# Optimization experiments

Measured on AMD Instinct MI355X. Metric: run time of the kernel, lower is better.

The kernel has to match this reference:

```python
import jax, jax.numpy as jnp
import numpy as np
from jax import lax

L, B, N, D = 6, 4, 2048, 512
H, DH = 8, 64
ID = H * DH           # 512
M = 266               # int(64*log(64)) random features
INNER = 2 * D         # conformer expansion
K = 31                # depthwise kernel
PAD = (15, 15)        # calc_same_padding(31)
EPS_LN = 1e-5


def setup_inputs() -> dict:
    key = jax.random.key(0)
    ks = jax.random.split(key, 12)
    s = 0.02
    return {
        "x": jax.random.normal(ks[0], (B, N, D), jnp.float32),
        "ln1_g": jnp.ones((L, D), jnp.float32),
        "ln1_b": jnp.zeros((L, D), jnp.float32),
        "wq": jax.random.normal(ks[1], (L, ID, D), jnp.float32) * s,
        "bq": jnp.zeros((L, ID), jnp.float32),
        "wk": jax.random.normal(ks[2], (L, ID, D), jnp.float32) * s,
        "bk": jnp.zeros((L, ID), jnp.float32),
        "wv": jax.random.normal(ks[3], (L, ID, D), jnp.float32) * s,
        "bv": jnp.zeros((L, ID), jnp.float32),
        "wo": jax.random.normal(ks[4], (L, ID, D), jnp.float32) * s,
        "bo": jnp.zeros((L, D), jnp.float32),
        # FAVOR+ random projection buffer (gaussian orthogonal ~ iid gaussian rows)
        "proj": jax.random.normal(ks[5], (L, M, DH), jnp.float32),
        "ln2_g": jnp.ones((L, D), jnp.float32),
        "ln2_b": jnp.zeros((L, D), jnp.float32),
        "pw1_w": jax.random.normal(ks[6], (L, 2 * INNER, D), jnp.float32) * s,
        "pw1_b": jnp.zeros((L, 2 * INNER), jnp.float32),
        "dw_w": jax.random.normal(ks[7], (L, INNER, K), jnp.float32) * s,
        "dw_b": jnp.zeros((L, INNER), jnp.float32),
        "pw2_w": jax.random.normal(ks[8], (L, D, INNER), jnp.float32) * s,
        "pw2_b": jnp.zeros((L, D), jnp.float32),
    }


def layer_norm(x, g, b):
    mu = jnp.mean(x, axis=-1, keepdims=True)
    var = jnp.mean((x - mu) ** 2, axis=-1, keepdims=True)
    return (x - mu) * lax.rsqrt(var + EPS_LN) * g + b


def softmax_kernel(data, proj, is_query, eps=1e-4):
    # data: [b,h,n,dh], proj: [m,dh]
    dn = DH ** -0.25
    ratio = M ** -0.5
    data_dash = jnp.einsum('bhnd,md->bhnm', dn * data, proj)
    diag = jnp.sum(data * data, axis=-1, keepdims=True) * 0.5 * dn * dn  # [b,h,n,1]
    if is_query:
        mx = jnp.max(data_dash, axis=-1, keepdims=True)
        return ratio * (jnp.exp(data_dash - diag - mx) + eps)
    else:
        return ratio * jnp.exp(data_dash - diag + eps)


def favor_attention(q, k, v, proj):
    qp = softmax_kernel(q, proj, True)   # [b,h,n,m]
    kp = softmax_kernel(k, proj, False)  # [b,h,n,m]
    k_cumsum = jnp.sum(kp, axis=-2)      # [b,h,m]
    d_inv = 1.0 / (jnp.einsum('bhnm,bhm->bhn', qp, k_cumsum) + 1e-8)
    context = jnp.einsum('bhnm,bhne->bhme', kp, v)          # [b,h,m,dh]
    out = jnp.einsum('bhme,bhnm,bhn->bhne', context, qp, d_inv)
    return out


def pcmer_forward(x, ln1_g, ln1_b, wq, bq, wk, bk, wv, bv, wo, bo, proj,
                  ln2_g, ln2_b, pw1_w, pw1_b, dw_w, dw_b, pw2_w, pw2_b):
    for l in range(L):
        # --- self attention (FAVOR+) ---
        h = layer_norm(x, ln1_g[l], ln1_b[l])
        q = (h @ wq[l].T + bq[l]).reshape(B, N, H, DH).transpose(0, 2, 1, 3)
        k = (h @ wk[l].T + bk[l]).reshape(B, N, H, DH).transpose(0, 2, 1, 3)
        v = (h @ wv[l].T + bv[l]).reshape(B, N, H, DH).transpose(0, 2, 1, 3)
        o = favor_attention(q, k, v, proj[l])                 # [b,h,n,dh]
        o = o.transpose(0, 2, 1, 3).reshape(B, N, ID)
        x = x + (o @ wo[l].T + bo[l])
        # --- conformer conv module ---
        h = layer_norm(x, ln2_g[l], ln2_b[l])
        y = h @ pw1_w[l].T + pw1_b[l]                         # [b,n,2*inner]
        a, g = y[..., :INNER], y[..., INNER:]
        y = a * jax.nn.sigmoid(g)                             # GLU
        yt = jnp.pad(y.transpose(0, 2, 1), ((0, 0), (0, 0), PAD))  # [b,inner,n+30]
        dw = lax.conv_general_dilated(
            yt, dw_w[l][:, None, :], window_strides=(1,), padding='VALID',
            feature_group_count=INNER,
            dimension_numbers=('NCH', 'OIH', 'NCH')) + dw_b[l][None, :, None]
        dw = jax.nn.silu(dw).transpose(0, 2, 1)               # [b,n,inner]
        x = x + (dw @ pw2_w[l].T + pw2_b[l])
    return x


def reference(x, ln1_g, ln1_b, wq, bq, wk, bk, wv, bv, wo, bo, proj,
              ln2_g, ln2_b, pw1_w, pw1_b, dw_w, dw_b, pw2_w, pw2_b):
    return pcmer_forward(x, ln1_g, ln1_b, wq, bq, wk, bk, wv, bv, wo, bo, proj,
                         ln2_g, ln2_b, pw1_w, pw1_b, dw_w, dw_b, pw2_w, pw2_b)
```

## Files before the change

kernel.cpp:

```cpp
#include <hip/hip_runtime.h>


#define L_LAYERS 6
#define B_ 4
#define N_ 2048
#define D_ 512
#define H_ 8
#define DH_ 64
#define M_ 266
#define INNER_ 1024
#define T_ 8192
#define PS_ 320
#define QKVS_ 1536
#define NS_ 8

typedef __attribute__((ext_vector_type(8))) short short8;
typedef __attribute__((ext_vector_type(4))) float floatx4;

__device__ __forceinline__ ushort f2bf(float f) {
  union { float f; uint u; } v; v.f = f;
  uint r = v.u + 0x7fffu + ((v.u >> 16) & 1u);
  return (ushort)(r >> 16);
}
__device__ __forceinline__ float bf2f(ushort u) {
  union { uint u; float f; } v; v.u = ((uint)u) << 16;
  return v.f;
}
__device__ __forceinline__ float wave_sum(float v) {
#pragma unroll
  for (int m = 1; m < 64; m <<= 1) v += __shfl_xor(v, m);
  return v;
}
__device__ __forceinline__ void async_cp16(const void* g, void* l) {
  __builtin_amdgcn_global_load_lds(
      (const __attribute__((address_space(1))) void*)g,
      (__attribute__((address_space(3))) void*)l, 16, 0, 0);
}

__global__ void f2bf4_kernel(const float4* __restrict__ in, ushort* __restrict__ out, int n4) {
  int i = blockIdx.x * 256 + threadIdx.x;
  if (i < n4) {
    float4 v = in[i];
    ushort4 r;
    r.x = f2bf(v.x); r.y = f2bf(v.y); r.z = f2bf(v.z); r.w = f2bf(v.w);
    *(ushort4*)(out + (size_t)i * 4) = r;
  }
}
__global__ void pack_qkv_w(const float4* __restrict__ src, ushort* __restrict__ dst, int off) {
  int i = blockIdx.x * 256 + threadIdx.x;
  if (i >= L_LAYERS * 512 * 128) return;
  int l = i >> 16;
  int rem = i & 65535;
  int row = rem >> 7, c4 = rem & 127;
  float4 v = src[i];
  ushort4 r;
  r.x = f2bf(v.x); r.y = f2bf(v.y); r.z = f2bf(v.z); r.w = f2bf(v.w);
  *(ushort4*)(dst + ((size_t)l * QKVS_ + off + row) * 512 + c4 * 4) = r;
}
__global__ void pack_qkv_b(const float* __restrict__ bq, const float* __restrict__ bk,
                           const float* __restrict__ bv, float* __restrict__ dst) {
  int i = blockIdx.x * 256 + threadIdx.x;
  if (i >= L_LAYERS * QKVS_) return;
  int l = i / QKVS_, c = i % QKVS_;
  dst[i] = c < 512 ? bq[l * 512 + c] : (c < 1024 ? bk[l * 512 + c - 512] : bv[l * 512 + c - 1024]);
}
__global__ void pad_proj(const float* __restrict__ proj, ushort* __restrict__ dst) {
  int i = blockIdx.x * 256 + threadIdx.x;
  if (i >= L_LAYERS * 320 * 64) return;
  int l = i / (320 * 64), rem = i % (320 * 64), m = rem >> 6, kk = rem & 63;
  dst[i] = (m < M_) ? f2bf(proj[((size_t)l * M_ + m) * 64 + kk]) : (ushort)0;
}
__global__ void pack_pw1_w(const float4* __restrict__ src, ushort* __restrict__ dst) {
  int i = blockIdx.x * 256 + threadIdx.x;
  if (i >= L_LAYERS * 2048 * 128) return;
  int l = i >> 18;
  int rem = i & 262143;
  int cp = rem >> 7, c4 = rem & 127;
  int s = (cp >> 4) & 1;
  int srow = ((cp >> 5) << 4) + (cp & 15) + s * 1024;
  float4 v = src[((size_t)l * 2048 + srow) * 128 + c4];
  ushort4 r;
  r.x = f2bf(v.x); r.y = f2bf(v.y); r.z = f2bf(v.z); r.w = f2bf(v.w);
  *(ushort4*)(dst + ((size_t)l * 2048 + cp) * 512 + c4 * 4) = r;
}
__global__ void pack_pw1_b(const float* __restrict__ src, float* __restrict__ dst) {
  int i = blockIdx.x * 256 + threadIdx.x;
  if (i >= L_LAYERS * 2048) return;
  int l = i >> 11, cp = i & 2047;
  int s = (cp >> 4) & 1;
  int srow = ((cp >> 5) << 4) + (cp & 15) + s * 1024;
  dst[i] = src[l * 2048 + srow];
}

__global__ __launch_bounds__(256) void ln_kernel(const float* __restrict__ x,
                                                 const float* __restrict__ g,
                                                 const float* __restrict__ b,
                                                 ushort* __restrict__ out) {
  const int t = blockIdx.x;
  const int tid = threadIdx.x;
  const float* row = x + (size_t)t * D_;
  float v0 = row[tid], v1 = row[tid + 256];
  float s1 = v0 + v1;
  float s2 = v0 * v0 + v1 * v1;
  s1 = wave_sum(s1);
  s2 = wave_sum(s2);
  __shared__ float sh1[4], sh2[4];
  int w = tid >> 6;
  if ((tid & 63) == 0) { sh1[w] = s1; sh2[w] = s2; }
  __syncthreads();
  s1 = sh1[0] + sh1[1] + sh1[2] + sh1[3];
  s2 = sh2[0] + sh2[1] + sh2[2] + sh2[3];
  float mu = s1 * (1.f / D_);
  float var = s2 * (1.f / D_) - mu * mu;
  float rs = rsqrtf(var + 1e-5f);
  out[(size_t)t * D_ + tid]       = f2bf((v0 - mu) * rs * g[tid] + b[tid]);
  out[(size_t)t * D_ + tid + 256] = f2bf((v1 - mu) * rs * g[tid + 256] + b[tid + 256]);
}

template <bool HAS_RES, bool OUT_BF16, int ACT, int KT>
__global__ __launch_bounds__(256) void gemm_mfma(const ushort* __restrict__ A,
                                                 const ushort* __restrict__ W,
                                                 const float* __restrict__ bias,
                                                 const float* __restrict__ res,
                                                 void* __restrict__ Cout,
                                                 int ldc) {
  constexpr int NT = KT / 32;
  __shared__ ushort As[3][128 * 32];
  __shared__ ushort Bs[3][128 * 32];
  const int tid = threadIdx.x;
  const int w = tid >> 6, lane = tid & 63;
  const int row0 = blockIdx.x * 128, col0 = blockIdx.y * 128;
  const int rl = lane >> 2;
  const int lc = ((lane & 3) ^ ((lane >> 3) & 3)) * 8;
  const ushort* gA0 = A + (size_t)(row0 + w * 32 + rl) * KT + lc;
  const ushort* gA1 = gA0 + (size_t)16 * KT;
  const ushort* gB0 = W + (size_t)(col0 + w * 32 + rl) * KT + lc;
  const ushort* gB1 = gB0 + (size_t)16 * KT;
  const int m16 = lane & 15, quad = lane >> 4;
  const int awr = (w >> 1) * 64, bwc = (w & 1) * 64;
  floatx4 acc[4][4] = {};

  auto stage = [&](int t, int buf) {
    async_cp16(gA0 + t * 32, As[buf] + w * 1024);
    async_cp16(gA1 + t * 32, As[buf] + w * 1024 + 512);
    async_cp16(gB0 + t * 32, Bs[buf] + w * 1024);
    async_cp16(gB1 + t * 32, Bs[buf] + w * 1024 + 512);
  };
  auto body = [&](int buf, bool bar2) {
    short8 af[4], bfr[4];
#pragma unroll
    for (int i = 0; i < 4; i++) {
      int r = awr + i * 16 + m16;
      af[i] = *(const short8*)&As[buf][r * 32 + (quad ^ ((r >> 1) & 3)) * 8];
    }
#pragma unroll
    for (int j = 0; j < 4; j++) {
      int r = bwc + j * 16 + m16;
      bfr[j] = *(const short8*)&Bs[buf][r * 32 + (quad ^ ((r >> 1) & 3)) * 8];
    }
    if (bar2) {
      asm volatile("s_waitcnt lgkmcnt(0)" ::: "memory");
      __builtin_amdgcn_sched_barrier(0);
      __builtin_amdgcn_s_barrier();
    }
#pragma unroll
    for (int i = 0; i < 4; i++)
#pragma unroll
      for (int j = 0; j < 4; j++)
        acc[i][j] = __builtin_amdgcn_mfma_f32_16x16x32_bf16(af[i], bfr[j], acc[i][j], 0, 0, 0);
  };

  stage(0, 0);
  stage(1, 1);
  int c = 0;
  for (int t = 0; t < NT - 2; t++) {
    int pf = c + 2; if (pf >= 3) pf -= 3;
    stage(t + 2, pf);
    asm volatile("s_waitcnt vmcnt(8)" ::: "memory");
    __builtin_amdgcn_s_barrier();
    body(c, true);
    c++; if (c >= 3) c -= 3;
  }
  asm volatile("s_waitcnt vmcnt(4)" ::: "memory");
  __builtin_amdgcn_s_barrier();
  body(c, false);
  c++; if (c >= 3) c -= 3;
  asm volatile("s_waitcnt vmcnt(0)" ::: "memory");
  __builtin_amdgcn_s_barrier();
  body(c, false);

  if (ACT == 0) {
#pragma unroll
    for (int i = 0; i < 4; i++) {
      const int r0 = row0 + awr + i * 16 + quad * 4;
#pragma unroll
      for (int j = 0; j < 4; j++) {
        const int cc = col0 + bwc + j * 16 + m16;
        const float bv = bias[cc];
#pragma unroll
        for (int r = 0; r < 4; r++) {
          float vv = acc[i][j][r] + bv;
          if (HAS_RES) vv += res[(size_t)(r0 + r) * ldc + cc];
          if (OUT_BF16) ((ushort*)Cout)[(size_t)(r0 + r) * ldc + cc] = f2bf(vv);
          else          ((float*)Cout)[(size_t)(r0 + r) * ldc + cc] = vv;
        }
      }
    }
  } else {
#pragma unroll
    for (int i = 0; i < 4; i++) {
      const int r0 = row0 + awr + i * 16 + quad * 4;
#pragma unroll
      for (int jp = 0; jp < 2; jp++) {
        const int j = jp * 2;
        const int ca = col0 + bwc + j * 16 + m16;
        const float ba = bias[ca], bg = bias[ca + 16];
        const int oc = ((col0 + bwc) >> 1) + jp * 16 + m16;
#pragma unroll
        for (int r = 0; r < 4; r++) {
          float a = acc[i][j][r] + ba;
          float g = acc[i][j + 1][r] + bg;
          float z = a / (1.f + expf(-g));
          ((ushort*)Cout)[(size_t)(r0 + r) * ldc + oc] = f2bf(z);
        }
      }
    }
  }
}

template <bool OUT_BF16, int ACT, int KT>
__global__ __launch_bounds__(256, 2) void gemm_big(const ushort* __restrict__ A,
                                                   const ushort* __restrict__ W,
                                                   const float* __restrict__ bias,
                                                   void* __restrict__ Cout,
                                                   int ldc) {
  constexpr int NT = KT / 32;
  __shared__ ushort As[3][256 * 32];
  __shared__ ushort Bs[3][128 * 32];
  const int tid = threadIdx.x;
  const int w = tid >> 6, lane = tid & 63;
  const int row0 = blockIdx.x * 256, col0 = blockIdx.y * 128;
  const int rl = lane >> 2;
  const int lc = ((lane & 3) ^ ((lane >> 3) & 3)) * 8;
  const ushort* gA = A + (size_t)(row0 + w * 64 + rl) * KT + lc;
  const ushort* gB = W + (size_t)(col0 + w * 32 + rl) * KT + lc;
  const int m16 = lane & 15, quad = lane >> 4;
  const int awr = (w >> 1) * 128;
  const int bwc = (w & 1) * 64;
  floatx4 acc[8][4] = {};

  auto stage = [&](int t, int buf) {
#pragma unroll
    for (int j = 0; j < 4; j++)
      async_cp16(gA + ((size_t)j * 16) * KT + t * 32, As[buf] + w * 2048 + j * 512);
#pragma unroll
    for (int j = 0; j < 2; j++)
      async_cp16(gB + ((size_t)j * 16) * KT + t * 32, Bs[buf] + w * 1024 + j * 512);
  };
  auto body = [&](int buf, bool bar2) {
    short8 af[8], bfr[4];
#pragma unroll
    for (int i = 0; i < 8; i++) {
      int r = awr + i * 16 + m16;
      af[i] = *(const short8*)&As[buf][r * 32 + (quad ^ ((r >> 1) & 3)) * 8];
    }
#pragma unroll
    for (int j = 0; j < 4; j++) {
      int r = bwc + j * 16 + m16;
      bfr[j] = *(const short8*)&Bs[buf][r * 32 + (quad ^ ((r >> 1) & 3)) * 8];
    }
    if (bar2) {
      asm volatile("s_waitcnt lgkmcnt(0)" ::: "memory");
      __builtin_amdgcn_sched_barrier(0);
      __builtin_amdgcn_s_barrier();
    }
#pragma unroll
    for (int i = 0; i < 8; i++)
#pragma unroll
      for (int j = 0; j < 4; j++)
        acc[i][j] = __builtin_amdgcn_mfma_f32_16x16x32_bf16(af[i], bfr[j], acc[i][j], 0, 0, 0);
  };

  stage(0, 0);
  stage(1, 1);
  int c = 0;
  for (int t = 0; t < NT - 2; t++) {
    int pf = c + 2; if (pf >= 3) pf -= 3;
    stage(t + 2, pf);
    asm volatile("s_waitcnt vmcnt(12)" ::: "memory");
    __builtin_amdgcn_s_barrier();
    body(c, true);
    c++; if (c >= 3) c -= 3;
  }
  asm volatile("s_waitcnt vmcnt(6)" ::: "memory");
  __builtin_amdgcn_s_barrier();
  body(c, false);
  c++; if (c >= 3) c -= 3;
  asm volatile("s_waitcnt vmcnt(0)" ::: "memory");
  __builtin_amdgcn_s_barrier();
  body(c, false);

  if (ACT == 0) {
#pragma unroll
    for (int i = 0; i < 8; i++) {
      const int r0 = row0 + awr + i * 16 + quad * 4;
#pragma unroll
      for (int j = 0; j < 4; j++) {
        const int cc = col0 + bwc + j * 16 + m16;
        const float bv = bias[cc];
#pragma unroll
        for (int r = 0; r < 4; r++) {
          float vv = acc[i][j][r] + bv;
          if (OUT_BF16) ((ushort*)Cout)[(size_t)(r0 + r) * ldc + cc] = f2bf(vv);
          else          ((float*)Cout)[(size_t)(r0 + r) * ldc + cc] = vv;
        }
      }
    }
  } else {
#pragma unroll
    for (int i = 0; i < 8; i++) {
      const int r0 = row0 + awr + i * 16 + quad * 4;
#pragma unroll
      for (int jp = 0; jp < 2; jp++) {
        const int j = jp * 2;
        const int ca = col0 + bwc + j * 16 + m16;
        const float ba = bias[ca], bg = bias[ca + 16];
        const int oc = ((col0 + bwc) >> 1) + jp * 16 + m16;
#pragma unroll
        for (int r = 0; r < 4; r++) {
          float a = acc[i][j][r] + ba;
          float g = acc[i][j + 1][r] + bg;
          float z = a / (1.f + expf(-g));
          ((ushort*)Cout)[(size_t)(r0 + r) * ldc + oc] = f2bf(z);
        }
      }
    }
  }
}

__global__ __launch_bounds__(256) void ctx_phi_mfma(const ushort* __restrict__ qkv,
                                                    const ushort* __restrict__ projp,
                                                    float* __restrict__ part,
                                                    float* __restrict__ kpart) {
  __shared__ ushort projs[64 * 64];
  __shared__ ushort kts[32 * 64];
  __shared__ ushort kps[64][40];
  __shared__ ushort vsT[64][40];
  __shared__ float diag_sh[32];
  __shared__ float kshare[4][64];
  const int bh = blockIdx.x, mt = blockIdx.y, ns = blockIdx.z;
  const int b = bh >> 3, h = bh & 7;
  const int m0 = mt * 64;
  const int tid = threadIdx.x;
  const int w = tid >> 6, lane = tid & 63, l16 = lane & 15, quad = lane >> 4;
  const int rl8 = lane >> 3;
  const int lc8 = ((lane & 7) ^ (rl8 & 7)) * 8;
#pragma unroll
  for (int j = 0; j < 2; j++) {
    const int rb = w * 16 + j * 8;
    async_cp16(projp + (size_t)(m0 + rb + rl8) * 64 + lc8, projs + rb * 64);
  }
  const int nn = tid >> 3;
  const int a8 = tid & 7;
  const int gn = nn >> 3, jn = nn & 7;
  const int pc = ((gn ^ (a8 & 3)) << 3) | jn;
  const int km = tid & 63, kg = tid >> 6;
  const float dn = 0.35355339059327373f;
  const float ratio = 0.06131393394849658f;
  floatx4 acc[4] = {};
  float ksp = 0.f;
  for (int nstep = 0; nstep < 2048 / NS_ / 32; nstep++) {
    const int n0 = ns * (2048 / NS_) + nstep * 32;
    {
      const int rb = w * 8;
      async_cp16(qkv + (size_t)(b * N_ + n0 + rb + rl8) * QKVS_ + 512 + h * 64 + lc8,
                 kts + rb * 64);
    }
    uint4 vv = *(const uint4*)(qkv + ((size_t)(b * N_ + n0 + nn)) * QKVS_ + 1024 + h * 64 + a8 * 8);
    __syncthreads();
    {
      const int r = tid >> 3;
      const int c = tid & 7;
      short8 kv8 = *(const short8*)&kts[r * 64 + c * 8];
      const ushort* u = (const ushort*)&kv8;
      float s = 0.f;
#pragma unroll
      for (int j = 0; j < 8; j++) { float f = bf2f(u[j]); s += f * f; }
      s += __shfl_xor(s, 1);
      s += __shfl_xor(s, 2);
      s += __shfl_xor(s, 4);
      if ((tid & 7) == 0) diag_sh[r] = 0.0625f * s;
    }
    {
      const ushort* ve = (const ushort*)&vv;
#pragma unroll
      for (int j = 0; j < 8; j++) vsT[a8 * 8 + j][pc] = ve[j];
    }
    __syncthreads();
    floatx4 pacc[2] = {};
#pragma unroll
    for (int s = 0; s < 2; s++) {
      const int ar = w * 16 + l16;
      short8 af = *(const short8*)&projs[ar * 64 + ((s * 4 + quad) ^ (ar & 7)) * 8];
#pragma unroll
      for (int nj = 0; nj < 2; nj++) {
        const int br = nj * 16 + l16;
        short8 bf = *(const short8*)&kts[br * 64 + ((s * 4 + quad) ^ (br & 7)) * 8];
        pacc[nj] = __builtin_amdgcn_mfma_f32_16x16x32_bf16(af, bf, pacc[nj], 0, 0, 0);
      }
    }
#pragma unroll
    for (int nj = 0; nj < 2; nj++) {
      const int n = nj * 16 + l16;
      const float dgn = diag_sh[n];
#pragma unroll
      for (int r = 0; r < 4; r++) {
        const int m = w * 16 + quad * 4 + r;
        float val = (m0 + m < M_) ? ratio * expf(dn * pacc[nj][r] - dgn + 1e-4f) : 0.f;
        kps[m][(((n >> 3) ^ ((m >> 3) & 3)) << 3) | (n & 7)] = f2bf(val);
      }
    }
    __syncthreads();
    const int am = w * 16 + l16;
    const int apg = quad ^ ((am >> 3) & 3);
    short8 af = *(const short8*)&kps[am][apg * 8];
#pragma unroll
    for (int et = 0; et < 4; et++) {
      const int be = et * 16 + l16;
      const int bpg = quad ^ ((be >> 3) & 3);
      short8 bf = *(const short8*)&vsT[be][bpg * 8];
      acc[et] = __builtin_amdgcn_mfma_f32_16x16x32_bf16(af, bf, acc[et], 0, 0, 0);
    }
    {
      short8 kr = *(const short8*)&kps[km][kg * 8];
      const ushort* ku = (const ushort*)&kr;
#pragma unroll
      for (int j = 0; j < 8; j++) ksp += bf2f(ku[j]);
    }
  }
  float* pb = part + ((size_t)(bh * NS_ + ns) * 5 + mt) * 4096;
#pragma unroll
  for (int et = 0; et < 4; et++)
#pragma unroll
    for (int r = 0; r < 4; r++)
      pb[(w * 16 + quad * 4 + r) * 64 + et * 16 + l16] = acc[et][r];
  kshare[kg][km] = ksp;
  __syncthreads();
  if (tid < 64)
    kpart[((size_t)(bh * NS_ + ns) * 5 + mt) * 64 + tid] =
        kshare[0][tid] + kshare[1][tid] + kshare[2][tid] + kshare[3][tid];
}

__global__ __launch_bounds__(256) void ctx_reduce(const float* __restrict__ part,
                                                  const float* __restrict__ kpart,
                                                  ushort* __restrict__ ctxbT,
                                                  float* __restrict__ ksum) {
  const int bh = blockIdx.x, mt = blockIdx.y;
  const int tid = threadIdx.x;
  const int w = tid >> 6, lane = tid & 63;
  for (int oc = w; oc < 8; oc += 4) {
    const int mbase = mt * 64 + oc * 8;
    if (mbase < 288) {
      float s[8] = {0.f, 0.f, 0.f, 0.f, 0.f, 0.f, 0.f, 0.f};
#pragma unroll
      for (int ns = 0; ns < NS_; ns++) {
        const float* pb = part + ((size_t)(bh * NS_ + ns) * 5 + mt) * 4096;
#pragma unroll
        for (int ml = 0; ml < 8; ml++) s[ml] += pb[(oc * 8 + ml) * 64 + lane];
      }
      ushort tmp[8];
#pragma unroll
      for (int ml = 0; ml < 8; ml++) tmp[ml] = f2bf(s[ml]);
      *(short8*)(ctxbT + ((size_t)(bh * 64 + lane)) * 288 + mbase) = *(const short8*)tmp;
    }
  }
  if (tid < 64) {
    float s = 0.f;
#pragma unroll
    for (int ns = 0; ns < NS_; ns++)
      s += kpart[((size_t)(bh * NS_ + ns) * 5 + mt) * 64 + tid];
    ksum[(size_t)bh * PS_ + mt * 64 + tid] = s;
  }
}

__global__ __launch_bounds__(256, 4) void attn_fused(const ushort* __restrict__ qkv,
                                                     const ushort* __restrict__ projp,
                                                     const ushort* __restrict__ ctxbT,
                                                     const float* __restrict__ ksum,
                                                     ushort* __restrict__ o) {
  __shared__ __align__(16) ushort sm[14336];
  __shared__ float ks_sh[288];
  __shared__ float diag_sh[64];
  ushort* As = sm;
  ushort* Bs = sm + 4096;
  ushort (*qst)[40] = (ushort(*)[40])sm;
  const int bh = blockIdx.x, b = bh >> 3, h = bh & 7;
  const int n0 = blockIdx.y * 64;
  const int tid = threadIdx.x;
  const int w = tid >> 6, lane = tid & 63, l16 = lane & 15, quad = lane >> 4;
  const int rl8 = lane >> 3;
  const int lc8 = ((lane & 7) ^ (rl8 & 7)) * 8;
#pragma unroll
  for (int j = 0; j < 2; j++) {
    const int rb = w * 16 + j * 8;
    async_cp16(qkv + (size_t)(b * N_ + n0 + rb + rl8) * QKVS_ + h * 64 + lc8, As + rb * 64);
  }
#pragma unroll
  for (int j = 0; j < 5; j++) {
    const int rb = w * 40 + j * 8;
    async_cp16(projp + (size_t)(rb + rl8) * 64 + lc8, Bs + rb * 64);
  }
  for (int i = tid; i < 288; i += 256) ks_sh[i] = ksum[(size_t)bh * PS_ + i];
  __syncthreads();
  {
    const int r = w * 16 + (lane >> 2);
    const int c0 = 2 * (lane & 3);
    float s = 0.f;
#pragma unroll
    for (int cc = 0; cc < 2; cc++) {
      short8 vv = *(const short8*)&As[r * 64 + ((c0 + cc) ^ (r & 7)) * 8];
      const ushort* u = (const ushort*)&vv;
#pragma unroll
      for (int j = 0; j < 8; j++) { float f = bf2f(u[j]); s += f * f; }
    }
    s += __shfl_xor(s, 1);
    s += __shfl_xor(s, 2);
    if ((lane & 3) == 0) diag_sh[r] = 0.0625f * s;
  }
  __syncthreads();
  float dgr[4];
#pragma unroll
  for (int r = 0; r < 4; r++) dgr[r] = diag_sh[w * 16 + quad * 4 + r];
  floatx4 acc[18];
#pragma unroll
  for (int cf = 0; cf < 18; cf++) acc[cf] = (floatx4){0.f, 0.f, 0.f, 0.f};
  const int ar = w * 16 + l16;
#pragma unroll
  for (int s = 0; s < 2; s++) {
    short8 af = *(const short8*)&As[ar * 64 + ((s * 4 + quad) ^ (ar & 7)) * 8];
#pragma unroll
    for (int cf = 0; cf < 10; cf++) {
      const int br = cf * 16 + l16;
      short8 bf = *(const short8*)&Bs[br * 64 + ((s * 4 + quad) ^ (br & 7)) * 8];
      acc[cf] = __builtin_amdgcn_mfma_f32_16x16x32_bf16(af, bf, acc[cf], 0, 0, 0);
    }
  }
  __syncthreads();
#pragma unroll
  for (int j = 0; j < 4; j++) {
    const int rb = w * 32 + j * 8;
    async_cp16(projp + (size_t)(160 + rb + rl8) * 64 + lc8, Bs + rb * 64);
  }
  __syncthreads();
#pragma unroll
  for (int s = 0; s < 2; s++) {
    short8 af = *(const short8*)&As[ar * 64 + ((s * 4 + quad) ^ (ar & 7)) * 8];
#pragma unroll
    for (int cf = 10; cf < 18; cf++) {
      const int br = (cf - 10) * 16 + l16;
      short8 bf = *(const short8*)&Bs[br * 64 + ((s * 4 + quad) ^ (br & 7)) * 8];
      acc[cf] = __builtin_amdgcn_mfma_f32_16x16x32_bf16(af, bf, acc[cf], 0, 0, 0);
    }
  }
  const float dn = 0.35355339059327373f;
  const float ratio = 0.06131393394849658f;
  float mxr[4];
#pragma unroll
  for (int r = 0; r < 4; r++) {
    float mx = -1e30f;
#pragma unroll
    for (int cf = 0; cf < 18; cf++) {
      const int col = cf * 16 + l16;
      if (col < M_) mx = fmaxf(mx, dn * acc[cf][r]);
    }
    mx = fmaxf(mx, __shfl_xor(mx, 1));
    mx = fmaxf(mx, __shfl_xor(mx, 2));
    mx = fmaxf(mx, __shfl_xor(mx, 4));
    mx = fmaxf(mx, __shfl_xor(mx, 8));
    mxr[r] = mx;
  }
  __syncthreads();
  float dacc[4] = {0.f, 0.f, 0.f, 0.f};
  floatx4 acc2[4] = {};
  const ushort* ctxrow = ctxbT + (size_t)bh * (64 * 288);
  for (int m0 = 0; m0 < 288; m0 += 32) {
    const int cf0 = m0 >> 4;
#pragma unroll
    for (int cc = 0; cc < 2; cc++) {
      const int col = m0 + cc * 16 + l16;
      const float kv = ks_sh[col];
#pragma unroll
      for (int r = 0; r < 4; r++) {
        float val = (col < M_) ? ratio * (expf(dn * acc[cf0 + cc][r] - dgr[r] - mxr[r]) + 1e-4f)
                               : 0.f;
        qst[w * 16 + quad * 4 + r][cc * 16 + l16] = f2bf(val);
        dacc[r] += val * kv;
      }
    }
    short8 af = *(const short8*)&qst[w * 16 + l16][quad * 8];
#pragma unroll
    for (int et = 0; et < 4; et++) {
      short8 bf = *(const short8*)(ctxrow + (size_t)(et * 16 + l16) * 288 + m0 + quad * 8);
      acc2[et] = __builtin_amdgcn_mfma_f32_16x16x32_bf16(af, bf, acc2[et], 0, 0, 0);
    }
  }
  float di[4];
#pragma unroll
  for (int r = 0; r < 4; r++) {
    float d = dacc[r];
    d += __shfl_xor(d, 1);
    d += __shfl_xor(d, 2);
    d += __shfl_xor(d, 4);
    d += __shfl_xor(d, 8);
    di[r] = 1.f / (d + 1e-8f);
  }
#pragma unroll
  for (int r = 0; r < 4; r++) {
    const int n = n0 + w * 16 + quad * 4 + r;
#pragma unroll
    for (int et = 0; et < 4; et++)
      o[((size_t)(b * N_ + n)) * 512 + h * 64 + et * 16 + l16] = f2bf(acc2[et][r] * di[r]);
  }
}

#define TN_ 32
__global__ __launch_bounds__(256) void dwconv_kernel(const ushort* __restrict__ x,
                                                     const float* __restrict__ w,
                                                     const float* __restrict__ bias,
                                                     ushort* __restrict__ out) {
  const int bid = blockIdx.x;
  const int cb = bid & 3;
  const int nb = (bid >> 2) & (N_ / TN_ - 1);
  const int b  = bid >> 8;
  const int c = cb * 256 + threadIdx.x;
  const int n0 = nb * TN_;
  float win[TN_ + 30];
#pragma unroll
  for (int i = 0; i < TN_ + 30; i++) {
    int nn = n0 + i - 15;
    win[i] = (nn >= 0 && nn < N_) ? bf2f(x[(size_t)(b * N_ + nn) * INNER_ + c]) : 0.f;
  }
  float wc[31];
#pragma unroll
  for (int kk = 0; kk < 31; kk++) wc[kk] = w[c * 31 + kk];
  const float bsv = bias[c];
#pragma unroll
  for (int j = 0; j < TN_; j++) {
    float acc = bsv;
#pragma unroll
    for (int kk = 0; kk < 31; kk++) acc += win[j + kk] * wc[kk];
    acc = acc / (1.f + expf(-acc));
    out[(size_t)(b * N_ + n0 + j) * INNER_ + c] = f2bf(acc);
  }
}

extern "C" void kernel_launch(void* const* d_in, const int* in_sizes, int n_in,
                              void* d_out, int out_size, void* d_ws, size_t ws_size,
                              hipStream_t stream) {
  const float* in_x  = (const float*)d_in[0];
  const float* ln1_g = (const float*)d_in[1];
  const float* ln1_b = (const float*)d_in[2];
  const float* wq    = (const float*)d_in[3];
  const float* bq    = (const float*)d_in[4];
  const float* wk    = (const float*)d_in[5];
  const float* bk    = (const float*)d_in[6];
  const float* wv    = (const float*)d_in[7];
  const float* bv    = (const float*)d_in[8];
  const float* wo    = (const float*)d_in[9];
  const float* bo    = (const float*)d_in[10];
  const float* proj  = (const float*)d_in[11];
  const float* ln2_g = (const float*)d_in[12];
  const float* ln2_b = (const float*)d_in[13];
  const float* pw1_w = (const float*)d_in[14];
  const float* pw1_b = (const float*)d_in[15];
  const float* dw_w  = (const float*)d_in[16];
  const float* dw_b  = (const float*)d_in[17];
  const float* pw2_w = (const float*)d_in[18];
  const float* pw2_b = (const float*)d_in[19];

  char* cur = (char*)d_ws;
  auto alloc = [&](size_t bytes) { char* p = cur; cur += (bytes + 255) & ~(size_t)255; return p; };
  float*  x    = (float*)alloc((size_t)T_ * D_ * 4);
  ushort* p    = (ushort*)alloc((size_t)T_ * INNER_ * 2 * 2);
  float*  part = (float*)alloc((size_t)32 * NS_ * 5 * 4096 * 4);
  float*  kpart= (float*)alloc((size_t)32 * NS_ * 5 * 64 * 4);
  ushort* ctxb = (ushort*)alloc((size_t)32 * 288 * 64 * 2);
  float*  ksum = (float*)alloc((size_t)32 * PS_ * 4);
  ushort* h    = (ushort*)alloc((size_t)T_ * D_ * 2);
  ushort* qkv  = (ushort*)alloc((size_t)T_ * QKVS_ * 2);
  ushort* obuf = (ushort*)alloc((size_t)T_ * D_ * 2);
  ushort* wqkv_b = (ushort*)alloc((size_t)L_LAYERS * QKVS_ * 512 * 2);
  float*  bqkv   = (float*)alloc((size_t)L_LAYERS * QKVS_ * 4);
  ushort* wo_b = (ushort*)alloc((size_t)L_LAYERS * D_ * D_ * 2);
  ushort* pjp  = (ushort*)alloc((size_t)L_LAYERS * 320 * 64 * 2);
  ushort* p1_b = (ushort*)alloc((size_t)L_LAYERS * 2048 * D_ * 2);
  float*  pb1  = (float*)alloc((size_t)L_LAYERS * 2048 * 4);
  ushort* p2_b = (ushort*)alloc((size_t)L_LAYERS * D_ * INNER_ * 2);
  ushort* glu  = p;
  ushort* conv = p + (size_t)T_ * INNER_;

  pack_qkv_w<<<(L_LAYERS * 512 * 128 + 255) / 256, 256, 0, stream>>>((const float4*)wq, wqkv_b, 0);
  pack_qkv_w<<<(L_LAYERS * 512 * 128 + 255) / 256, 256, 0, stream>>>((const float4*)wk, wqkv_b, 512);
  pack_qkv_w<<<(L_LAYERS * 512 * 128 + 255) / 256, 256, 0, stream>>>((const float4*)wv, wqkv_b, 1024);
  pack_qkv_b<<<(L_LAYERS * QKVS_ + 255) / 256, 256, 0, stream>>>(bq, bk, bv, bqkv);
  pad_proj<<<(L_LAYERS * 320 * 64 + 255) / 256, 256, 0, stream>>>(proj, pjp);
  pack_pw1_w<<<(L_LAYERS * 2048 * 128 + 255) / 256, 256, 0, stream>>>((const float4*)pw1_w, p1_b);
  pack_pw1_b<<<(L_LAYERS * 2048 + 255) / 256, 256, 0, stream>>>(pw1_b, pb1);
  {
    int n4 = L_LAYERS * D_ * D_ / 4;
    f2bf4_kernel<<<(n4 + 255) / 256, 256, 0, stream>>>((const float4*)wo, wo_b, n4);
    n4 = L_LAYERS * D_ * INNER_ / 4;
    f2bf4_kernel<<<(n4 + 255) / 256, 256, 0, stream>>>((const float4*)pw2_w, p2_b, n4);
  }

  for (int l = 0; l < L_LAYERS; l++) {
    const ushort* wqkvl = wqkv_b + (size_t)l * QKVS_ * 512;
    const ushort* wol = wo_b + (size_t)l * D_ * D_;
    const ushort* pjl = pjp + (size_t)l * 320 * 64;
    const ushort* p1l = p1_b + (size_t)l * 2048 * D_;
    const ushort* p2l = p2_b + (size_t)l * D_ * INNER_;
    const float*  dwl = dw_w + (size_t)l * INNER_ * 31;
    const float*  dwbl = dw_b + (size_t)l * INNER_;
    const float*  xin = (l == 0) ? in_x : x;
    float* xout = (l == L_LAYERS - 1) ? (float*)d_out : x;

    ln_kernel<<<T_, 256, 0, stream>>>(xin, ln1_g + l * D_, ln1_b + l * D_, h);
    gemm_big<true, 0, 512><<<dim3(T_ / 256, QKVS_ / 128), 256, 0, stream>>>(
        h, wqkvl, bqkv + (size_t)l * QKVS_, qkv, QKVS_);
    ctx_phi_mfma<<<dim3(32, 5, NS_), 256, 0, stream>>>(qkv, pjl, part, kpart);
    ctx_reduce<<<dim3(32, 5), 256, 0, stream>>>(part, kpart, ctxb, ksum);
    attn_fused<<<dim3(32, 32), 256, 0, stream>>>(qkv, pjl, ctxb, ksum, obuf);
    gemm_mfma<true, false, 0, 512><<<dim3(T_ / 128, 4), 256, 0, stream>>>(
        obuf, wol, bo + l * D_, xin, x, D_);
    ln_kernel<<<T_, 256, 0, stream>>>(x, ln2_g + l * D_, ln2_b + l * D_, h);
    gemm_big<true, 1, 512><<<dim3(T_ / 256, 16), 256, 0, stream>>>(
        h, p1l, pb1 + (size_t)l * 2048, glu, INNER_);
    dwconv_kernel<<<B_ * (N_ / TN_) * 4, 256, 0, stream>>>(glu, dwl, dwbl, conv);
    gemm_mfma<true, false, 0, 1024><<<dim3(T_ / 128, 4), 256, 0, stream>>>(
        conv, p2l, pw2_b + l * D_, x, xout, D_);
  }
}
```

Measured before the change: 1.225 ms.

## Use smaller-tile GEMM for N=512 outputs, XCD swizzle, setprio, fused packing kernels

```diff
diff --git a/kernel.cpp b/kernel.cpp
--- a/kernel.cpp
+++ b/kernel.cpp
@@ -36,39 +36,59 @@
       (const __attribute__((address_space(1))) void*)g,
       (__attribute__((address_space(3))) void*)l, 16, 0, 0);
 }
-
-__global__ void f2bf4_kernel(const float4* __restrict__ in, ushort* __restrict__ out, int n4) {
+__device__ __forceinline__ int xcd_swz(int bid, int n) {
+  return (bid & 7) * (n >> 3) + (bid >> 3);
+}
+
+__global__ void f2bf4_dual(const float4* __restrict__ s1, int n1,
+                           const float4* __restrict__ s2, int n2,
+                           ushort* __restrict__ out) {
   int i = blockIdx.x * 256 + threadIdx.x;
-  if (i < n4) {
-    float4 v = in[i];
-    ushort4 r;
-    r.x = f2bf(v.x); r.y = f2bf(v.y); r.z = f2bf(v.z); r.w = f2bf(v.w);
-    *(ushort4*)(out + (size_t)i * 4) = r;
-  }
-}
-__global__ void pack_qkv_w(const float4* __restrict__ src, ushort* __restrict__ dst, int off) {
-  int i = blockIdx.x * 256 + threadIdx.x;
-  if (i >= L_LAYERS * 512 * 128) return;
-  int l = i >> 16;
-  int rem = i & 65535;
-  int row = rem >> 7, c4 = rem & 127;
-  float4 v = src[i];
+  if (i >= n1 + n2) return;
+  float4 v = (i < n1) ? s1[i] : s2[i - n1];
   ushort4 r;
   r.x = f2bf(v.x); r.y = f2bf(v.y); r.z = f2bf(v.z); r.w = f2bf(v.w);
-  *(ushort4*)(dst + ((size_t)l * QKVS_ + off + row) * 512 + c4 * 4) = r;
-}
-__global__ void pack_qkv_b(const float* __restrict__ bq, const float* __restrict__ bk,
-                           const float* __restrict__ bv, float* __restrict__ dst) {
+  *(ushort4*)(out + (size_t)i * 4) = r;
+}
+__global__ void pack_qkv_w3(const float4* __restrict__ wq, const float4* __restrict__ wk,
+                            const float4* __restrict__ wv, ushort* __restrict__ dst) {
   int i = blockIdx.x * 256 + threadIdx.x;
-  if (i >= L_LAYERS * QKVS_) return;
-  int l = i / QKVS_, c = i % QKVS_;
-  dst[i] = c < 512 ? bq[l * 512 + c] : (c < 1024 ? bk[l * 512 + c - 512] : bv[l * 512 + c - 1024]);
-}
-__global__ void pad_proj(const float* __restrict__ proj, ushort* __restrict__ dst) {
+  const int per = L_LAYERS * 512 * 128;
+  if (i >= 3 * per) return;
+  int seg = i / per;
+  int rem = i - seg * per;
+  const float4* src = seg == 0 ? wq : (seg == 1 ? wk : wv);
+  int l = rem >> 16;
+  int r2 = rem & 65535;
+  int row = r2 >> 7, c4 = r2 & 127;
+  float4 v = src[rem];
+  ushort4 r;
+  r.x = f2bf(v.x); r.y = f2bf(v.y); r.z = f2bf(v.z); r.w = f2bf(v.w);
+  *(ushort4*)(dst + ((size_t)l * QKVS_ + seg * 512 + row) * 512 + c4 * 4) = r;
+}
+__global__ void pack_small(const float* __restrict__ bq, const float* __restrict__ bk,
+                           const float* __restrict__ bv, float* __restrict__ bqkv,
+                           const float* __restrict__ proj, ushort* __restrict__ pjp,
+                           const float* __restrict__ pw1b, float* __restrict__ pb1) {
   int i = blockIdx.x * 256 + threadIdx.x;
-  if (i >= L_LAYERS * 320 * 64) return;
-  int l = i / (320 * 64), rem = i % (320 * 64), m = rem >> 6, kk = rem & 63;
-  dst[i] = (m < M_) ? f2bf(proj[((size_t)l * M_ + m) * 64 + kk]) : (ushort)0;
+  const int A = L_LAYERS * QKVS_;
+  const int Bn = L_LAYERS * 320 * 64;
+  const int C = L_LAYERS * 2048;
+  if (i < A) {
+    int l = i / QKVS_, c = i % QKVS_;
+    bqkv[i] = c < 512 ? bq[l * 512 + c]
+                      : (c < 1024 ? bk[l * 512 + c - 512] : bv[l * 512 + c - 1024]);
+  } else if (i < A + Bn) {
+    int j = i - A;
+    int l = j / (320 * 64), rem = j % (320 * 64), m = rem >> 6, kk = rem & 63;
+    pjp[j] = (m < M_) ? f2bf(proj[((size_t)l * M_ + m) * 64 + kk]) : (ushort)0;
+  } else if (i < A + Bn + C) {
+    int j = i - A - Bn;
+    int l = j >> 11, cp = j & 2047;
+    int s = (cp >> 4) & 1;
+    int srow = ((cp >> 5) << 4) + (cp & 15) + s * 1024;
+    pb1[j] = pw1b[l * 2048 + srow];
+  }
 }
 __global__ void pack_pw1_w(const float4* __restrict__ src, ushort* __restrict__ dst) {
   int i = blockIdx.x * 256 + threadIdx.x;
@@ -82,14 +102,6 @@
   ushort4 r;
   r.x = f2bf(v.x); r.y = f2bf(v.y); r.z = f2bf(v.z); r.w = f2bf(v.w);
   *(ushort4*)(dst + ((size_t)l * 2048 + cp) * 512 + c4 * 4) = r;
-}
-__global__ void pack_pw1_b(const float* __restrict__ src, float* __restrict__ dst) {
-  int i = blockIdx.x * 256 + threadIdx.x;
-  if (i >= L_LAYERS * 2048) return;
-  int l = i >> 11, cp = i & 2047;
-  int s = (cp >> 4) & 1;
-  int srow = ((cp >> 5) << 4) + (cp & 15) + s * 1024;
-  dst[i] = src[l * 2048 + srow];
 }
 
 __global__ __launch_bounds__(256) void ln_kernel(const float* __restrict__ x,
@@ -117,117 +129,6 @@
   out[(size_t)t * D_ + tid + 256] = f2bf((v1 - mu) * rs * g[tid + 256] + b[tid + 256]);
 }
 
-template <bool HAS_RES, bool OUT_BF16, int ACT, int KT>
-__global__ __launch_bounds__(256) void gemm_mfma(const ushort* __restrict__ A,
-                                                 const ushort* __restrict__ W,
-                                                 const float* __restrict__ bias,
-                                                 const float* __restrict__ res,
-                                                 void* __restrict__ Cout,
-                                                 int ldc) {
-  constexpr int NT = KT / 32;
-  __shared__ ushort As[3][128 * 32];
-  __shared__ ushort Bs[3][128 * 32];
-  const int tid = threadIdx.x;
-  const int w = tid >> 6, lane = tid & 63;
-  const int row0 = blockIdx.x * 128, col0 = blockIdx.y * 128;
-  const int rl = lane >> 2;
-  const int lc = ((lane & 3) ^ ((lane >> 3) & 3)) * 8;
-  const ushort* gA0 = A + (size_t)(row0 + w * 32 + rl) * KT + lc;
-  const ushort* gA1 = gA0 + (size_t)16 * KT;
-  const ushort* gB0 = W + (size_t)(col0 + w * 32 + rl) * KT + lc;
-  const ushort* gB1 = gB0 + (size_t)16 * KT;
-  const int m16 = lane & 15, quad = lane >> 4;
-  const int awr = (w >> 1) * 64, bwc = (w & 1) * 64;
-  floatx4 acc[4][4] = {};
-
-  auto stage = [&](int t, int buf) {
-    async_cp16(gA0 + t * 32, As[buf] + w * 1024);
-    async_cp16(gA1 + t * 32, As[buf] + w * 1024 + 512);
-    async_cp16(gB0 + t * 32, Bs[buf] + w * 1024);
-    async_cp16(gB1 + t * 32, Bs[buf] + w * 1024 + 512);
-  };
-  auto body = [&](int buf, bool bar2) {
-    short8 af[4], bfr[4];
-#pragma unroll
-    for (int i = 0; i < 4; i++) {
-      int r = awr + i * 16 + m16;
-      af[i] = *(const short8*)&As[buf][r * 32 + (quad ^ ((r >> 1) & 3)) * 8];
-    }
-#pragma unroll
-    for (int j = 0; j < 4; j++) {
-      int r = bwc + j * 16 + m16;
-      bfr[j] = *(const short8*)&Bs[buf][r * 32 + (quad ^ ((r >> 1) & 3)) * 8];
-    }
-    if (bar2) {
-      asm volatile("s_waitcnt lgkmcnt(0)" ::: "memory");
-      __builtin_amdgcn_sched_barrier(0);
-      __builtin_amdgcn_s_barrier();
-    }
-#pragma unroll
-    for (int i = 0; i < 4; i++)
-#pragma unroll
-      for (int j = 0; j < 4; j++)
-        acc[i][j] = __builtin_amdgcn_mfma_f32_16x16x32_bf16(af[i], bfr[j], acc[i][j], 0, 0, 0);
-  };
-
-  stage(0, 0);
-  stage(1, 1);
-  int c = 0;
-  for (int t = 0; t < NT - 2; t++) {
-    int pf = c + 2; if (pf >= 3) pf -= 3;
-    stage(t + 2, pf);
-    asm volatile("s_waitcnt vmcnt(8)" ::: "memory");
-    __builtin_amdgcn_s_barrier();
-    body(c, true);
-    c++; if (c >= 3) c -= 3;
-  }
-  asm volatile("s_waitcnt vmcnt(4)" ::: "memory");
-  __builtin_amdgcn_s_barrier();
-  body(c, false);
-  c++; if (c >= 3) c -= 3;
-  asm volatile("s_waitcnt vmcnt(0)" ::: "memory");
-  __builtin_amdgcn_s_barrier();
-  body(c, false);
-
-  if (ACT == 0) {
-#pragma unroll
-    for (int i = 0; i < 4; i++) {
-      const int r0 = row0 + awr + i * 16 + quad * 4;
-#pragma unroll
-      for (int j = 0; j < 4; j++) {
-        const int cc = col0 + bwc + j * 16 + m16;
-        const float bv = bias[cc];
-#pragma unroll
-        for (int r = 0; r < 4; r++) {
-          float vv = acc[i][j][r] + bv;
-          if (HAS_RES) vv += res[(size_t)(r0 + r) * ldc + cc];
-          if (OUT_BF16) ((ushort*)Cout)[(size_t)(r0 + r) * ldc + cc] = f2bf(vv);
-          else          ((float*)Cout)[(size_t)(r0 + r) * ldc + cc] = vv;
-        }
-      }
-    }
-  } else {
-#pragma unroll
-    for (int i = 0; i < 4; i++) {
-      const int r0 = row0 + awr + i * 16 + quad * 4;
-#pragma unroll
-      for (int jp = 0; jp < 2; jp++) {
-        const int j = jp * 2;
-        const int ca = col0 + bwc + j * 16 + m16;
-        const float ba = bias[ca], bg = bias[ca + 16];
-        const int oc = ((col0 + bwc) >> 1) + jp * 16 + m16;
-#pragma unroll
-        for (int r = 0; r < 4; r++) {
-          float a = acc[i][j][r] + ba;
-          float g = acc[i][j + 1][r] + bg;
-          float z = a / (1.f + expf(-g));
-          ((ushort*)Cout)[(size_t)(r0 + r) * ldc + oc] = f2bf(z);
-        }
-      }
-    }
-  }
-}
-
 template <bool OUT_BF16, int ACT, int KT>
 __global__ __launch_bounds__(256, 2) void gemm_big(const ushort* __restrict__ A,
                                                    const ushort* __restrict__ W,
@@ -239,7 +140,7 @@
   __shared__ ushort Bs[3][128 * 32];
   const int tid = threadIdx.x;
   const int w = tid >> 6, lane = tid & 63;
-  const int row0 = blockIdx.x * 256, col0 = blockIdx.y * 128;
+  const int row0 = xcd_swz(blockIdx.x, gridDim.x) * 256, col0 = blockIdx.y * 128;
   const int rl = lane >> 2;
   const int lc = ((lane & 3) ^ ((lane >> 3) & 3)) * 8;
   const ushort* gA = A + (size_t)(row0 + w * 64 + rl) * KT + lc;
@@ -274,11 +175,13 @@
       __builtin_amdgcn_sched_barrier(0);
       __builtin_amdgcn_s_barrier();
     }
+    __builtin_amdgcn_s_setprio(1);
 #pragma unroll
     for (int i = 0; i < 8; i++)
 #pragma unroll
       for (int j = 0; j < 4; j++)
         acc[i][j] = __builtin_amdgcn_mfma_f32_16x16x32_bf16(af[i], bfr[j], acc[i][j], 0, 0, 0);
+    __builtin_amdgcn_s_setprio(0);
   };
 
   stage(0, 0);
@@ -338,6 +241,94 @@
   }
 }
 
+template <int KT>
+__global__ __launch_bounds__(256, 4) void gemm_small(const ushort* __restrict__ A,
+                                                     const ushort* __restrict__ W,
+                                                     const float* __restrict__ bias,
+                                                     const float* __restrict__ res,
+                                                     float* __restrict__ Cout,
+                                                     int ldc) {
+  constexpr int NT = KT / 32;
+  __shared__ ushort As[3][64 * 32];
+  __shared__ ushort Bs[3][128 * 32];
+  const int tid = threadIdx.x;
+  const int w = tid >> 6, lane = tid & 63;
+  const int row0 = xcd_swz(blockIdx.x, gridDim.x) * 64, col0 = blockIdx.y * 128;
+  const int rl = lane >> 2;
+  const int lc = ((lane & 3) ^ ((lane >> 3) & 3)) * 8;
+  const ushort* gA = A + (size_t)(row0 + w * 16 + rl) * KT + lc;
+  const ushort* gB0 = W + (size_t)(col0 + w * 32 + rl) * KT + lc;
+  const ushort* gB1 = gB0 + (size_t)16 * KT;
+  const int m16 = lane & 15, quad = lane >> 4;
+  const int awr = (w >> 1) * 32;
+  const int bwc = (w & 1) * 64;
+  floatx4 acc[2][4] = {};
+
+  auto stage = [&](int t, int buf) {
+    async_cp16(gA + t * 32, As[buf] + w * 512);
+    async_cp16(gB0 + t * 32, Bs[buf] + w * 1024);
+    async_cp16(gB1 + t * 32, Bs[buf] + w * 1024 + 512);
+  };
+  auto body = [&](int buf, bool bar2) {
+    short8 af[2], bfr[4];
+#pragma unroll
+    for (int i = 0; i < 2; i++) {
+      int r = awr + i * 16 + m16;
+      af[i] = *(const short8*)&As[buf][r * 32 + (quad ^ ((r >> 1) & 3)) * 8];
+    }
+#pragma unroll
+    for (int j = 0; j < 4; j++) {
+      int r = bwc + j * 16 + m16;
+      bfr[j] = *(const short8*)&Bs[buf][r * 32 + (quad ^ ((r >> 1) & 3)) * 8];
+    }
+    if (bar2) {
+      asm volatile("s_waitcnt lgkmcnt(0)" ::: "memory");
+      __builtin_amdgcn_sched_barrier(0);
+      __builtin_amdgcn_s_barrier();
+    }
+    __builtin_amdgcn_s_setprio(1);
+#pragma unroll
+    for (int i = 0; i < 2; i++)
+#pragma unroll
+      for (int j = 0; j < 4; j++)
+        acc[i][j] = __builtin_amdgcn_mfma_f32_16x16x32_bf16(af[i], bfr[j], acc[i][j], 0, 0, 0);
+    __builtin_amdgcn_s_setprio(0);
+  };
+
+  stage(0, 0);
+  stage(1, 1);
+  int c = 0;
+  for (int t = 0; t < NT - 2; t++) {
+    int pf = c + 2; if (pf >= 3) pf -= 3;
+    stage(t + 2, pf);
+    asm volatile("s_waitcnt vmcnt(6)" ::: "memory");
+    __builtin_amdgcn_s_barrier();
+    body(c, true);
+    c++; if (c >= 3) c -= 3;
+  }
+  asm volatile("s_waitcnt vmcnt(3)" ::: "memory");
+  __builtin_amdgcn_s_barrier();
+  body(c, false);
+  c++; if (c >= 3) c -= 3;
+  asm volatile("s_waitcnt vmcnt(0)" ::: "memory");
+  __builtin_amdgcn_s_barrier();
+  body(c, false);
+
+#pragma unroll
+  for (int i = 0; i < 2; i++) {
+    const int r0 = row0 + awr + i * 16 + quad * 4;
+#pragma unroll
+    for (int j = 0; j < 4; j++) {
+      const int cc = col0 + bwc + j * 16 + m16;
+      const float bv = bias[cc];
+#pragma unroll
+      for (int r = 0; r < 4; r++)
+        Cout[(size_t)(r0 + r) * ldc + cc] =
+            acc[i][j][r] + bv + res[(size_t)(r0 + r) * ldc + cc];
+    }
+  }
+}
+
 __global__ __launch_bounds__(256) void ctx_phi_mfma(const ushort* __restrict__ qkv,
                                                     const ushort* __restrict__ projp,
                                                     float* __restrict__ part,
@@ -348,7 +339,7 @@
   __shared__ ushort vsT[64][40];
   __shared__ float diag_sh[32];
   __shared__ float kshare[4][64];
-  const int bh = blockIdx.x, mt = blockIdx.y, ns = blockIdx.z;
+  const int bh = xcd_swz(blockIdx.x, 32), mt = blockIdx.y, ns = blockIdx.z;
   const int b = bh >> 3, h = bh & 7;
   const int m0 = mt * 64;
   const int tid = threadIdx.x;
@@ -398,6 +389,7 @@
     }
     __syncthreads();
     floatx4 pacc[2] = {};
+    __builtin_amdgcn_s_setprio(1);
 #pragma unroll
     for (int s = 0; s < 2; s++) {
       const int ar = w * 16 + l16;
@@ -409,6 +401,7 @@
         pacc[nj] = __builtin_amdgcn_mfma_f32_16x16x32_bf16(af, bf, pacc[nj], 0, 0, 0);
       }
     }
+    __builtin_amdgcn_s_setprio(0);
 #pragma unroll
     for (int nj = 0; nj < 2; nj++) {
       const int n = nj * 16 + l16;
@@ -424,6 +417,7 @@
     const int am = w * 16 + l16;
     const int apg = quad ^ ((am >> 3) & 3);
     short8 af = *(const short8*)&kps[am][apg * 8];
+    __builtin_amdgcn_s_setprio(1);
 #pragma unroll
     for (int et = 0; et < 4; et++) {
       const int be = et * 16 + l16;
@@ -431,6 +425,7 @@
       short8 bf = *(const short8*)&vsT[be][bpg * 8];
       acc[et] = __builtin_amdgcn_mfma_f32_16x16x32_bf16(af, bf, acc[et], 0, 0, 0);
     }
+    __builtin_amdgcn_s_setprio(0);
     {
       short8 kr = *(const short8*)&kps[km][kg * 8];
       const ushort* ku = (const ushort*)&kr;
@@ -494,7 +489,7 @@
   ushort* As = sm;
   ushort* Bs = sm + 4096;
   ushort (*qst)[40] = (ushort(*)[40])sm;
-  const int bh = blockIdx.x, b = bh >> 3, h = bh & 7;
+  const int bh = xcd_swz(blockIdx.x, 32), b = bh >> 3, h = bh & 7;
   const int n0 = blockIdx.y * 64;
   const int tid = threadIdx.x;
   const int w = tid >> 6, lane = tid & 63, l16 = lane & 15, quad = lane >> 4;
@@ -535,6 +530,7 @@
 #pragma unroll
   for (int cf = 0; cf < 18; cf++) acc[cf] = (floatx4){0.f, 0.f, 0.f, 0.f};
   const int ar = w * 16 + l16;
+  __builtin_amdgcn_s_setprio(1);
 #pragma unroll
   for (int s = 0; s < 2; s++) {
     short8 af = *(const short8*)&As[ar * 64 + ((s * 4 + quad) ^ (ar & 7)) * 8];
@@ -545,6 +541,7 @@
       acc[cf] = __builtin_amdgcn_mfma_f32_16x16x32_bf16(af, bf, acc[cf], 0, 0, 0);
     }
   }
+  __builtin_amdgcn_s_setprio(0);
   __syncthreads();
 #pragma unroll
   for (int j = 0; j < 4; j++) {
@@ -552,6 +549,7 @@
     async_cp16(projp + (size_t)(160 + rb + rl8) * 64 + lc8, Bs + rb * 64);
   }
   __syncthreads();
+  __builtin_amdgcn_s_setprio(1);
 #pragma unroll
   for (int s = 0; s < 2; s++) {
     short8 af = *(const short8*)&As[ar * 64 + ((s * 4 + quad) ^ (ar & 7)) * 8];
@@ -562,6 +560,7 @@
       acc[cf] = __builtin_amdgcn_mfma_f32_16x16x32_bf16(af, bf, acc[cf], 0, 0, 0);
     }
   }
+  __builtin_amdgcn_s_setprio(0);
   const float dn = 0.35355339059327373f;
   const float ratio = 0.06131393394849658f;
   float mxr[4];
@@ -598,11 +597,13 @@
       }
     }
     short8 af = *(const short8*)&qst[w * 16 + l16][quad * 8];
+    __builtin_amdgcn_s_setprio(1);
 #pragma unroll
     for (int et = 0; et < 4; et++) {
       short8 bf = *(const short8*)(ctxrow + (size_t)(et * 16 + l16) * 288 + m0 + quad * 8);
       acc2[et] = __builtin_amdgcn_mfma_f32_16x16x32_bf16(af, bf, acc2[et], 0, 0, 0);
     }
+    __builtin_amdgcn_s_setprio(0);
   }
   float di[4];
 #pragma unroll
@@ -691,26 +692,26 @@
   ushort* obuf = (ushort*)alloc((size_t)T_ * D_ * 2);
   ushort* wqkv_b = (ushort*)alloc((size_t)L_LAYERS * QKVS_ * 512 * 2);
   float*  bqkv   = (float*)alloc((size_t)L_LAYERS * QKVS_ * 4);
-  ushort* wo_b = (ushort*)alloc((size_t)L_LAYERS * D_ * D_ * 2);
+  ushort* wo_b = (ushort*)alloc((size_t)L_LAYERS * D_ * D_ * 2 + (size_t)L_LAYERS * D_ * INNER_ * 2);
+  ushort* p2_b = wo_b + (size_t)L_LAYERS * D_ * D_;
   ushort* pjp  = (ushort*)alloc((size_t)L_LAYERS * 320 * 64 * 2);
   ushort* p1_b = (ushort*)alloc((size_t)L_LAYERS * 2048 * D_ * 2);
   float*  pb1  = (float*)alloc((size_t)L_LAYERS * 2048 * 4);
-  ushort* p2_b = (ushort*)alloc((size_t)L_LAYERS * D_ * INNER_ * 2);
   ushort* glu  = p;
   ushort* conv = p + (size_t)T_ * INNER_;
 
-  pack_qkv_w<<<(L_LAYERS * 512 * 128 + 255) / 256, 256, 0, stream>>>((const float4*)wq, wqkv_b, 0);
-  pack_qkv_w<<<(L_LAYERS * 512 * 128 + 255) / 256, 256, 0, stream>>>((const float4*)wk, wqkv_b, 512);
-  pack_qkv_w<<<(L_LAYERS * 512 * 128 + 255) / 256, 256, 0, stream>>>((const float4*)wv, wqkv_b, 1024);
-  pack_qkv_b<<<(L_LAYERS * QKVS_ + 255) / 256, 256, 0, stream>>>(bq, bk, bv, bqkv);
-  pad_proj<<<(L_LAYERS * 320 * 64 + 255) / 256, 256, 0, stream>>>(proj, pjp);
+  pack_qkv_w3<<<(3 * L_LAYERS * 512 * 128 + 255) / 256, 256, 0, stream>>>(
+      (const float4*)wq, (const float4*)wk, (const float4*)wv, wqkv_b);
   pack_pw1_w<<<(L_LAYERS * 2048 * 128 + 255) / 256, 256, 0, stream>>>((const float4*)pw1_w, p1_b);
-  pack_pw1_b<<<(L_LAYERS * 2048 + 255) / 256, 256, 0, stream>>>(pw1_b, pb1);
   {
-    int n4 = L_LAYERS * D_ * D_ / 4;
-    f2bf4_kernel<<<(n4 + 255) / 256, 256, 0, stream>>>((const float4*)wo, wo_b, n4);
-    n4 = L_LAYERS * D_ * INNER_ / 4;
-    f2bf4_kernel<<<(n4 + 255) / 256, 256, 0, stream>>>((const float4*)pw2_w, p2_b, n4);
+    int n1 = L_LAYERS * D_ * D_ / 4;
+    int n2 = L_LAYERS * D_ * INNER_ / 4;
+    f2bf4_dual<<<(n1 + n2 + 255) / 256, 256, 0, stream>>>(
+        (const float4*)wo, n1, (const float4*)pw2_w, n2, wo_b);
+  }
+  {
+    int tot = L_LAYERS * QKVS_ + L_LAYERS * 320 * 64 + L_LAYERS * 2048;
+    pack_small<<<(tot + 255) / 256, 256, 0, stream>>>(bq, bk, bv, bqkv, proj, pjp, pw1_b, pb1);
   }
 
   for (int l = 0; l < L_LAYERS; l++) {
@@ -730,13 +731,13 @@
     ctx_phi_mfma<<<dim3(32, 5, NS_), 256, 0, stream>>>(qkv, pjl, part, kpart);
     ctx_reduce<<<dim3(32, 5), 256, 0, stream>>>(part, kpart, ctxb, ksum);
     attn_fused<<<dim3(32, 32), 256, 0, stream>>>(qkv, pjl, ctxb, ksum, obuf);
-    gemm_mfma<true, false, 0, 512><<<dim3(T_ / 128, 4), 256, 0, stream>>>(
+    gemm_small<512><<<dim3(T_ / 64, 4), 256, 0, stream>>>(
         obuf, wol, bo + l * D_, xin, x, D_);
     ln_kernel<<<T_, 256, 0, stream>>>(x, ln2_g + l * D_, ln2_b + l * D_, h);
     gemm_big<true, 1, 512><<<dim3(T_ / 256, 16), 256, 0, stream>>>(
         h, p1l, pb1 + (size_t)l * 2048, glu, INNER_);
     dwconv_kernel<<<B_ * (N_ / TN_) * 4, 256, 0, stream>>>(glu, dwl, dwbl, conv);
-    gemm_mfma<true, false, 0, 1024><<<dim3(T_ / 128, 4), 256, 0, stream>>>(
+    gemm_small<1024><<<dim3(T_ / 64, 4), 256, 0, stream>>>(
         conv, p2l, pw2_b + l * D_, x, xout, D_);
   }
 }
```

Result: slower. 1.249 ms (+2.0%).
